# Optimization experiments

Hardware: AMD Instinct MI355X
Metric: run time of the kernel (lower is better)

## Reference

```python
import jax, jax.numpy as jnp
import numpy as np

B = 32768
T = 1024  # num_time_bins


def setup_inputs() -> dict:
    key = jax.random.key(0)
    k1, k2, k3, k4 = jax.random.split(key, 4)
    hazard_values = jax.random.uniform(k1, (B, T), dtype=jnp.float32)
    labels_Y = jax.random.uniform(k2, (B,), dtype=jnp.float32) * T
    # nn.Linear(T, T): weight [T, T] (out, in), bias [T]
    lim = 1.0 / np.sqrt(T)
    W = jax.random.uniform(k3, (T, T), minval=-lim, maxval=lim, dtype=jnp.float32)
    b = jax.random.uniform(k4, (T,), minval=-lim, maxval=lim, dtype=jnp.float32)
    return {"hazard_values": hazard_values, "labels_Y": labels_Y, "W": W, "b": b}


def reference(hazard_values, labels_Y, W, b):
    # linear + sigmoid + argmax -> per-row truncation position
    logits = hazard_values @ W.T + b                       # [B, T]
    trunc_pos = jnp.argmax(jax.nn.sigmoid(logits), axis=1, keepdims=True)  # [B, 1] int
    # survival curve
    S = jnp.cumprod(1.0 - hazard_values, axis=1)           # [B, T]
    # vectorized truncation decay: for t >= p, multiply by exp(-(t - p))
    t = jnp.arange(T)[None, :]                             # [1, T]
    decay = jnp.where(t >= trunc_pos,
                      jnp.exp(-(t - trunc_pos).astype(S.dtype)),
                      jnp.ones((), S.dtype))
    S = S * decay
    # MSE between argmax position and labels (original prints; we skip prints)
    p = trunc_pos[:, 0].astype(jnp.float32)
    truncation_loss = jnp.mean((p - labels_Y) ** 2)
    return trunc_pos, S, truncation_loss
```

## Files before the change

kernel.cpp:

```cpp
#include <hip/hip_runtime.h>

#define B_ROWS 32768
#define T_BINS 1024

typedef __attribute__((ext_vector_type(8))) _Float16 half8;
typedef __attribute__((ext_vector_type(4))) float floatx4;

__device__ __forceinline__ unsigned long long pack_max(float v, int col) {
    unsigned x = __float_as_uint(v);
    x = (x & 0x80000000u) ? ~x : (x | 0x80000000u);
    return ((unsigned long long)x << 32) | (unsigned)(~col);
}

__device__ __forceinline__ void async16(const _Float16* g, _Float16* l) {
    __builtin_amdgcn_global_load_lds(
        (const __attribute__((address_space(1))) unsigned int*)g,
        (__attribute__((address_space(3))) unsigned int*)l,
        16, 0, 0);
}

__global__ __launch_bounds__(256) void tof16_kernel(
    const float* __restrict__ src, _Float16* __restrict__ dst, int n4)
{
    int idx = blockIdx.x * 256 + threadIdx.x;
    if (idx >= n4) return;
    float4 x = ((const float4*)src)[idx];
    union { _Float16 h[4]; ushort4 u; } cv;
    cv.h[0] = (_Float16)x.x;
    cv.h[1] = (_Float16)x.y;
    cv.h[2] = (_Float16)x.z;
    cv.h[3] = (_Float16)x.w;
    ((ushort4*)dst)[idx] = cv.u;
}

__global__ __launch_bounds__(256) void gemm_f16_argmax(
    const _Float16* __restrict__ Ag, const _Float16* __restrict__ Wg,
    const float* __restrict__ bias, unsigned long long* __restrict__ rec)
{
    __shared__ _Float16 sA[128 * 32];
    __shared__ _Float16 sW[128 * 32];

    const int tid  = threadIdx.x;
    const int lane = tid & 63;
    const int wv   = tid >> 6;
    const int wr   = wv >> 1;
    const int wc   = wv & 1;
    const int bx   = blockIdx.x;
    const int by   = blockIdx.y;

    floatx4 acc[4][4];
#pragma unroll
    for (int i = 0; i < 4; ++i)
#pragma unroll
        for (int j = 0; j < 4; ++j) acc[i][j] = (floatx4){0.f, 0.f, 0.f, 0.f};

    const int c0 = tid, c1 = 256 + tid;
    const int r0 = c0 >> 2, kc0 = (c0 & 3) * 8;
    const int r1 = c1 >> 2, kc1 = (c1 & 3) * 8;
    const int ub0 = (wv * 64) * 8;
    const int ub1 = (256 + wv * 64) * 8;

    const size_t a0 = (size_t)(by * 128 + r0) * T_BINS + kc0;
    const size_t a1 = (size_t)(by * 128 + r1) * T_BINS + kc1;
    const size_t w0 = (size_t)(bx * 128 + r0) * T_BINS + kc0;
    const size_t w1 = (size_t)(bx * 128 + r1) * T_BINS + kc1;

    const int ko = (lane >> 4) * 8;

    for (int k0 = 0; k0 < T_BINS; k0 += 32) {
        async16(Ag + a0 + k0, &sA[ub0]);
        async16(Ag + a1 + k0, &sA[ub1]);
        async16(Wg + w0 + k0, &sW[ub0]);
        async16(Wg + w1 + k0, &sW[ub1]);
        asm volatile("s_waitcnt vmcnt(0)" ::: "memory");
        __syncthreads();

        half8 ah[4], wh[4];
#pragma unroll
        for (int i = 0; i < 4; ++i) {
            int ra = (wr * 64 + i * 16 + (lane & 15)) * 32 + ko;
            int rw = (wc * 64 + i * 16 + (lane & 15)) * 32 + ko;
            ah[i] = *(const half8*)&sA[ra];
            wh[i] = *(const half8*)&sW[rw];
        }
#pragma unroll
        for (int i = 0; i < 4; ++i)
#pragma unroll
            for (int j = 0; j < 4; ++j)
                acc[i][j] = __builtin_amdgcn_mfma_f32_16x16x32_f16(ah[i], wh[j], acc[i][j], 0, 0, 0);
        __syncthreads();
    }

    const int colbase = bx * 128 + wc * 64 + (lane & 15);
    float bj[4];
#pragma unroll
    for (int j = 0; j < 4; ++j) bj[j] = bias[colbase + j * 16];

#pragma unroll
    for (int i = 0; i < 4; ++i) {
#pragma unroll
        for (int r = 0; r < 4; ++r) {
            float best = acc[i][0][r] + bj[0];
            int   bc   = colbase;
#pragma unroll
            for (int j = 1; j < 4; ++j) {
                float v = acc[i][j][r] + bj[j];
                if (v > best) { best = v; bc = colbase + j * 16; }
            }
#pragma unroll
            for (int off = 8; off >= 1; off >>= 1) {
                float ov = __shfl_xor(best, off, 64);
                int   oc = __shfl_xor(bc, off, 64);
                if (ov > best || (ov == best && oc < bc)) { best = ov; bc = oc; }
            }
            if ((lane & 15) == 0) {
                int rowG = by * 128 + wr * 64 + i * 16 + (lane >> 4) * 4 + r;
                atomicMax(&rec[rowG], pack_max(best, bc));
            }
        }
    }
}

#define BMf 64
#define BKf 16
#define LDSS (BMf + 4)
__global__ __launch_bounds__(256) void gemm_argmax_fp32(
    const float* __restrict__ A, const float* __restrict__ W,
    const float* __restrict__ bias, unsigned long long* __restrict__ rec)
{
    __shared__ float As[BKf][LDSS];
    __shared__ float Ws[BKf][LDSS];
    const int tid = threadIdx.x;
    const int tx = tid & 15, ty = tid >> 4;
    const int bx = blockIdx.x, by = blockIdx.y;
    const int ar = tid >> 2, ak = (tid & 3) << 2;
    const float* Arow = A + (size_t)(by * BMf + ar) * T_BINS + ak;
    const float* Wrow = W + (size_t)(bx * BMf + ar) * T_BINS + ak;
    float acc[4][4];
#pragma unroll
    for (int i = 0; i < 4; ++i)
#pragma unroll
        for (int j = 0; j < 4; ++j) acc[i][j] = 0.f;
    for (int k0 = 0; k0 < T_BINS; k0 += BKf) {
        float4 av = *(const float4*)(Arow + k0);
        float4 wvv = *(const float4*)(Wrow + k0);
        As[ak + 0][ar] = av.x; As[ak + 1][ar] = av.y; As[ak + 2][ar] = av.z; As[ak + 3][ar] = av.w;
        Ws[ak + 0][ar] = wvv.x; Ws[ak + 1][ar] = wvv.y; Ws[ak + 2][ar] = wvv.z; Ws[ak + 3][ar] = wvv.w;
        __syncthreads();
#pragma unroll
        for (int k = 0; k < BKf; ++k) {
            float4 a4 = *(const float4*)&As[k][ty * 4];
            float4 w4 = *(const float4*)&Ws[k][tx * 4];
            float aa[4] = {a4.x, a4.y, a4.z, a4.w};
            float ww[4] = {w4.x, w4.y, w4.z, w4.w};
#pragma unroll
            for (int i = 0; i < 4; ++i)
#pragma unroll
                for (int j = 0; j < 4; ++j) acc[i][j] = fmaf(aa[i], ww[j], acc[i][j]);
        }
        __syncthreads();
    }
    const int colBase = bx * BMf + tx * 4;
    float bv[4];
#pragma unroll
    for (int j = 0; j < 4; ++j) bv[j] = bias[colBase + j];
#pragma unroll
    for (int i = 0; i < 4; ++i) {
        float best = acc[i][0] + bv[0];
        int bc = colBase;
#pragma unroll
        for (int j = 1; j < 4; ++j) {
            float v = acc[i][j] + bv[j];
            if (v > best) { best = v; bc = colBase + j; }
        }
#pragma unroll
        for (int off = 8; off >= 1; off >>= 1) {
            float ov = __shfl_xor(best, off, 64);
            int oc = __shfl_xor(bc, off, 64);
            if (ov > best || (ov == best && oc < bc)) { best = ov; bc = oc; }
        }
        if (tx == 0) atomicMax(&rec[by * BMf + ty * 4 + i], pack_max(best, bc));
    }
}

__global__ __launch_bounds__(256) void finalize_kernel(
    const unsigned long long* __restrict__ rec, const float* __restrict__ labels,
    float* __restrict__ out_trunc, float* __restrict__ loss_acc)
{
    int i = blockIdx.x * 256 + threadIdx.x;
    unsigned col = ~(unsigned)(rec[i] & 0xFFFFFFFFull);
    float p = (float)col;
    out_trunc[i] = p;
    float d = p - labels[i];
    float term = d * d * (1.0f / (float)B_ROWS);
#pragma unroll
    for (int off = 32; off >= 1; off >>= 1)
        term += __shfl_down(term, off, 64);
    __shared__ float partials[4];
    int lane = threadIdx.x & 63, wv = threadIdx.x >> 6;
    if (lane == 0) partials[wv] = term;
    __syncthreads();
    if (threadIdx.x == 0)
        atomicAdd(loss_acc, partials[0] + partials[1] + partials[2] + partials[3]);
}

__global__ __launch_bounds__(256) void scan_kernel_f16(
    const _Float16* __restrict__ Hh, const float* __restrict__ trunc_f,
    float* __restrict__ Sout)
{
    const int row = blockIdx.x;
    const int tid = threadIdx.x;
    const int lane = tid & 63;
    const int wv = tid >> 6;

    union { ushort4 u; _Float16 h[4]; } cv;
    cv.u = ((const ushort4*)Hh)[(size_t)row * (T_BINS / 4) + tid];
    float l0 = 1.f - (float)cv.h[0];
    float l1 = l0 * (1.f - (float)cv.h[1]);
    float l2 = l1 * (1.f - (float)cv.h[2]);
    float l3 = l2 * (1.f - (float)cv.h[3]);

    float x = l3;
#pragma unroll
    for (int off = 1; off < 64; off <<= 1) {
        float o = __shfl_up(x, off, 64);
        if (lane >= off) x *= o;
    }
    float ex = __shfl_up(x, 1, 64);
    if (lane == 0) ex = 1.f;

    __shared__ float wtot[4];
    if (lane == 63) wtot[wv] = x;
    __syncthreads();
    float wpre = 1.f;
#pragma unroll
    for (int w = 0; w < 3; ++w)
        if (w < wv) wpre *= wtot[w];
    float pre = wpre * ex;

    int p = (int)trunc_f[row];
    int t0 = tid * 4;
    float sv[4] = {pre * l0, pre * l1, pre * l2, pre * l3};
#pragma unroll
    for (int j = 0; j < 4; ++j) {
        int t = t0 + j;
        if (t >= p) sv[j] *= __expf((float)(p - t));
    }
    float4 s4 = {sv[0], sv[1], sv[2], sv[3]};
    *(float4*)(Sout + (size_t)row * T_BINS + tid * 4) = s4;
}

__global__ __launch_bounds__(256) void scan_kernel_f32(
    const float* __restrict__ H, const float* __restrict__ trunc_f,
    float* __restrict__ Sout)
{
    const int row = blockIdx.x;
    const int tid = threadIdx.x;
    const int lane = tid & 63;
    const int wv = tid >> 6;
    const float4 h = *(const float4*)(H + (size_t)row * T_BINS + tid * 4);
    float l0 = 1.f - h.x;
    float l1 = l0 * (1.f - h.y);
    float l2 = l1 * (1.f - h.z);
    float l3 = l2 * (1.f - h.w);
    float x = l3;
#pragma unroll
    for (int off = 1; off < 64; off <<= 1) {
        float o = __shfl_up(x, off, 64);
        if (lane >= off) x *= o;
    }
    float ex = __shfl_up(x, 1, 64);
    if (lane == 0) ex = 1.f;
    __shared__ float wtot[4];
    if (lane == 63) wtot[wv] = x;
    __syncthreads();
    float wpre = 1.f;
#pragma unroll
    for (int w = 0; w < 3; ++w)
        if (w < wv) wpre *= wtot[w];
    float pre = wpre * ex;
    int p = (int)trunc_f[row];
    int t0 = tid * 4;
    float sv[4] = {pre * l0, pre * l1, pre * l2, pre * l3};
#pragma unroll
    for (int j = 0; j < 4; ++j) {
        int t = t0 + j;
        if (t >= p) sv[j] *= __expf((float)(p - t));
    }
    float4 s4 = {sv[0], sv[1], sv[2], sv[3]};
    *(float4*)(Sout + (size_t)row * T_BINS + tid * 4) = s4;
}

extern "C" void kernel_launch(void* const* d_in, const int* in_sizes, int n_in,
                              void* d_out, int out_size, void* d_ws, size_t ws_size,
                              hipStream_t stream)
{
    const float* hazard = (const float*)d_in[0];
    const float* labels = (const float*)d_in[1];
    const float* W      = (const float*)d_in[2];
    const float* bias   = (const float*)d_in[3];

    float* out       = (float*)d_out;
    float* out_trunc = out;
    float* out_S     = out + B_ROWS;
    float* out_loss  = out + B_ROWS + (size_t)B_ROWS * T_BINS;

    unsigned long long* rec = (unsigned long long*)out_S;

    hipMemsetAsync(rec, 0, (size_t)B_ROWS * sizeof(unsigned long long), stream);
    hipMemsetAsync(out_loss, 0, sizeof(float), stream);

    const size_t NA = (size_t)B_ROWS * T_BINS;
    const size_t NW = (size_t)T_BINS * T_BINS;
    const size_t need = (NA + NW) * sizeof(_Float16);

    if (ws_size >= need) {
        _Float16* Ah = (_Float16*)d_ws;
        _Float16* Wh = Ah + NA;
        tof16_kernel<<<(int)(NA / 4 / 256), 256, 0, stream>>>(hazard, Ah, (int)(NA / 4));
        tof16_kernel<<<(int)(NW / 4 / 256), 256, 0, stream>>>(W, Wh, (int)(NW / 4));
        dim3 ggrid(T_BINS / 128, B_ROWS / 128);
        gemm_f16_argmax<<<ggrid, 256, 0, stream>>>(Ah, Wh, bias, rec);
        finalize_kernel<<<B_ROWS / 256, 256, 0, stream>>>(rec, labels, out_trunc, out_loss);
        scan_kernel_f16<<<B_ROWS, 256, 0, stream>>>(Ah, out_trunc, out_S);
    } else {
        dim3 ggrid(T_BINS / BMf, B_ROWS / BMf);
        gemm_argmax_fp32<<<ggrid, 256, 0, stream>>>(hazard, W, bias, rec);
        finalize_kernel<<<B_ROWS / 256, 256, 0, stream>>>(rec, labels, out_trunc, out_loss);
        scan_kernel_f32<<<B_ROWS, 256, 0, stream>>>(hazard, out_trunc, out_S);
    }
}
```

Baseline: 386.1 us.

## Fuse fp16 GEMM, argmax, loss and survival scan into one mega kernel

Replaces the separate passes (fp32→fp16 conversion of hazard values, tiled GEMM with global atomicMax, finalize, and per-row scan) with one kernel per 64-row block. Each block converts its A tile to fp16 on the fly while streaming W, keeps a running argmax across all 1024 output columns, reduces it in shared memory, writes trunc/loss, then computes the cumprod and decay for its rows straight from fp32 hazard values. This removes the full fp16 copy of A, the record memset, global atomics and two extra launches. In exchange the grid is only 512 blocks with a serialized GEMM-then-scan inside each block, and A tiles are re-read once per column chunk, so occupancy and latency hiding may suffer.

```diff
diff --git a/kernel.cpp b/kernel.cpp
--- a/kernel.cpp
+++ b/kernel.cpp
@@ -12,7 +12,7 @@
     return ((unsigned long long)x << 32) | (unsigned)(~col);
 }
 
-__device__ __forceinline__ void async16(const _Float16* g, _Float16* l) {
+__device__ __forceinline__ void async16h(const _Float16* g, _Float16* l) {
     __builtin_amdgcn_global_load_lds(
         (const __attribute__((address_space(1))) unsigned int*)g,
         (__attribute__((address_space(3))) unsigned int*)l,
@@ -33,91 +33,169 @@
     ((ushort4*)dst)[idx] = cv.u;
 }
 
-__global__ __launch_bounds__(256) void gemm_f16_argmax(
-    const _Float16* __restrict__ Ag, const _Float16* __restrict__ Wg,
-    const float* __restrict__ bias, unsigned long long* __restrict__ rec)
-{
-    __shared__ _Float16 sA[128 * 32];
-    __shared__ _Float16 sW[128 * 32];
+__global__ __launch_bounds__(256, 2) void mega_kernel(
+    const float* __restrict__ A, const _Float16* __restrict__ Wh,
+    const float* __restrict__ bias, const float* __restrict__ labels,
+    float* __restrict__ out_trunc, float* __restrict__ out_S,
+    float* __restrict__ loss_acc)
+{
+    __shared__ _Float16 sA[64 * 32];
+    __shared__ _Float16 sW[256 * 32];
+    __shared__ unsigned long long cand[4][64];
+    __shared__ float trunc_s[64];
 
     const int tid  = threadIdx.x;
     const int lane = tid & 63;
-    const int wv   = tid >> 6;
-    const int wr   = wv >> 1;
-    const int wc   = wv & 1;
-    const int bx   = blockIdx.x;
-    const int by   = blockIdx.y;
-
-    floatx4 acc[4][4];
+    const int wc   = tid >> 6;
+    const int by   = blockIdx.x;
+
+    const int arow = tid >> 2;
+    const int akg  = (tid & 3) * 8;
+    const float* Abase = A + (size_t)(by * 64 + arow) * T_BINS + akg;
+    _Float16* sAdst = &sA[arow * 32 + akg];
+
+    const int ko = (lane >> 4) * 8;
+
+    float run_best[4][4];
+    int   run_col[4][4];
 #pragma unroll
     for (int i = 0; i < 4; ++i)
 #pragma unroll
-        for (int j = 0; j < 4; ++j) acc[i][j] = (floatx4){0.f, 0.f, 0.f, 0.f};
-
-    const int c0 = tid, c1 = 256 + tid;
-    const int r0 = c0 >> 2, kc0 = (c0 & 3) * 8;
-    const int r1 = c1 >> 2, kc1 = (c1 & 3) * 8;
-    const int ub0 = (wv * 64) * 8;
-    const int ub1 = (256 + wv * 64) * 8;
-
-    const size_t a0 = (size_t)(by * 128 + r0) * T_BINS + kc0;
-    const size_t a1 = (size_t)(by * 128 + r1) * T_BINS + kc1;
-    const size_t w0 = (size_t)(bx * 128 + r0) * T_BINS + kc0;
-    const size_t w1 = (size_t)(bx * 128 + r1) * T_BINS + kc1;
-
-    const int ko = (lane >> 4) * 8;
-
-    for (int k0 = 0; k0 < T_BINS; k0 += 32) {
-        async16(Ag + a0 + k0, &sA[ub0]);
-        async16(Ag + a1 + k0, &sA[ub1]);
-        async16(Wg + w0 + k0, &sW[ub0]);
-        async16(Wg + w1 + k0, &sW[ub1]);
-        asm volatile("s_waitcnt vmcnt(0)" ::: "memory");
-        __syncthreads();
-
-        half8 ah[4], wh[4];
-#pragma unroll
-        for (int i = 0; i < 4; ++i) {
-            int ra = (wr * 64 + i * 16 + (lane & 15)) * 32 + ko;
-            int rw = (wc * 64 + i * 16 + (lane & 15)) * 32 + ko;
-            ah[i] = *(const half8*)&sA[ra];
-            wh[i] = *(const half8*)&sW[rw];
-        }
+        for (int r = 0; r < 4; ++r) { run_best[i][r] = -3.4e38f; run_col[i][r] = 0; }
+
+    float4 pa0 = *(const float4*)(Abase);
+    float4 pa1 = *(const float4*)(Abase + 4);
+
+    for (int bx = 0; bx < 4; ++bx) {
+        const int colbase = bx * 256 + wc * 64 + (lane & 15);
+        float bj[4];
+#pragma unroll
+        for (int j = 0; j < 4; ++j) bj[j] = bias[colbase + j * 16];
+
+        floatx4 acc[4][4];
 #pragma unroll
         for (int i = 0; i < 4; ++i)
 #pragma unroll
+            for (int j = 0; j < 4; ++j) acc[i][j] = (floatx4){0.f, 0.f, 0.f, 0.f};
+
+        for (int k0 = 0; k0 < T_BINS; k0 += 32) {
+            half8 hv;
+            hv[0] = (_Float16)pa0.x; hv[1] = (_Float16)pa0.y;
+            hv[2] = (_Float16)pa0.z; hv[3] = (_Float16)pa0.w;
+            hv[4] = (_Float16)pa1.x; hv[5] = (_Float16)pa1.y;
+            hv[6] = (_Float16)pa1.z; hv[7] = (_Float16)pa1.w;
+            *(half8*)sAdst = hv;
+#pragma unroll
+            for (int r = 0; r < 4; ++r) {
+                int c = r * 256 + tid;
+                int wrow = c >> 2, wkc = (c & 3) * 8;
+                async16h(Wh + (size_t)(bx * 256 + wrow) * T_BINS + k0 + wkc,
+                         &sW[(r * 256 + wc * 64) * 8]);
+            }
+            int kn = (k0 + 32) & (T_BINS - 1);
+            pa0 = *(const float4*)(Abase + kn);
+            pa1 = *(const float4*)(Abase + kn + 4);
+            asm volatile("s_waitcnt vmcnt(0)" ::: "memory");
+            __syncthreads();
+            half8 ah[4], wh[4];
+#pragma unroll
+            for (int i = 0; i < 4; ++i)
+                ah[i] = *(const half8*)&sA[(i * 16 + (lane & 15)) * 32 + ko];
+#pragma unroll
             for (int j = 0; j < 4; ++j)
-                acc[i][j] = __builtin_amdgcn_mfma_f32_16x16x32_f16(ah[i], wh[j], acc[i][j], 0, 0, 0);
-        __syncthreads();
-    }
-
-    const int colbase = bx * 128 + wc * 64 + (lane & 15);
-    float bj[4];
-#pragma unroll
-    for (int j = 0; j < 4; ++j) bj[j] = bias[colbase + j * 16];
-
-#pragma unroll
-    for (int i = 0; i < 4; ++i) {
+                wh[j] = *(const half8*)&sW[(wc * 64 + j * 16 + (lane & 15)) * 32 + ko];
+#pragma unroll
+            for (int i = 0; i < 4; ++i)
+#pragma unroll
+                for (int j = 0; j < 4; ++j)
+                    acc[i][j] = __builtin_amdgcn_mfma_f32_16x16x32_f16(ah[i], wh[j], acc[i][j], 0, 0, 0);
+            __syncthreads();
+        }
+
+#pragma unroll
+        for (int i = 0; i < 4; ++i)
+#pragma unroll
+            for (int r = 0; r < 4; ++r)
+#pragma unroll
+                for (int j = 0; j < 4; ++j) {
+                    float v = acc[i][j][r] + bj[j];
+                    if (v > run_best[i][r]) { run_best[i][r] = v; run_col[i][r] = colbase + j * 16; }
+                }
+    }
+
+#pragma unroll
+    for (int i = 0; i < 4; ++i)
 #pragma unroll
         for (int r = 0; r < 4; ++r) {
-            float best = acc[i][0][r] + bj[0];
-            int   bc   = colbase;
-#pragma unroll
-            for (int j = 1; j < 4; ++j) {
-                float v = acc[i][j][r] + bj[j];
-                if (v > best) { best = v; bc = colbase + j * 16; }
-            }
+            float best = run_best[i][r];
+            int   bc   = run_col[i][r];
 #pragma unroll
             for (int off = 8; off >= 1; off >>= 1) {
                 float ov = __shfl_xor(best, off, 64);
                 int   oc = __shfl_xor(bc, off, 64);
                 if (ov > best || (ov == best && oc < bc)) { best = ov; bc = oc; }
             }
-            if ((lane & 15) == 0) {
-                int rowG = by * 128 + wr * 64 + i * 16 + (lane >> 4) * 4 + r;
-                atomicMax(&rec[rowG], pack_max(best, bc));
-            }
-        }
+            if ((lane & 15) == 0)
+                cand[wc][i * 16 + (lane >> 4) * 4 + r] = pack_max(best, bc);
+        }
+    __syncthreads();
+
+    if (tid < 64) {
+        unsigned long long m01 = cand[0][tid] > cand[1][tid] ? cand[0][tid] : cand[1][tid];
+        unsigned long long m23 = cand[2][tid] > cand[3][tid] ? cand[2][tid] : cand[3][tid];
+        unsigned long long m = m01 > m23 ? m01 : m23;
+        unsigned col = ~(unsigned)m;
+        float p = (float)col;
+        int rowG = by * 64 + tid;
+        out_trunc[rowG] = p;
+        trunc_s[tid] = p;
+        float d = p - labels[rowG];
+        float term = d * d * (1.0f / (float)B_ROWS);
+#pragma unroll
+        for (int off = 32; off >= 1; off >>= 1)
+            term += __shfl_down(term, off, 64);
+        if (tid == 0) atomicAdd(loss_acc, term);
+    }
+    __syncthreads();
+
+    for (int rr = 0; rr < 16; ++rr) {
+        int row  = wc * 16 + rr;
+        int rowG = by * 64 + row;
+        const float* Hrow = A + (size_t)rowG * T_BINS + lane * 16;
+        float4 h0 = *(const float4*)(Hrow + 0);
+        float4 h1 = *(const float4*)(Hrow + 4);
+        float4 h2 = *(const float4*)(Hrow + 8);
+        float4 h3 = *(const float4*)(Hrow + 12);
+        float hv[16] = {h0.x, h0.y, h0.z, h0.w, h1.x, h1.y, h1.z, h1.w,
+                        h2.x, h2.y, h2.z, h2.w, h3.x, h3.y, h3.z, h3.w};
+        float vprod[16];
+        float run = 1.f;
+#pragma unroll
+        for (int j = 0; j < 16; ++j) { run *= (1.f - hv[j]); vprod[j] = run; }
+        float x = run;
+#pragma unroll
+        for (int off = 1; off < 64; off <<= 1) {
+            float o = __shfl_up(x, off, 64);
+            if (lane >= off) x *= o;
+        }
+        float pre = __shfl_up(x, 1, 64);
+        if (lane == 0) pre = 1.f;
+
+        int p  = (int)trunc_s[row];
+        int t0 = lane * 16;
+        float sv[16];
+#pragma unroll
+        for (int j = 0; j < 16; ++j) {
+            float s = pre * vprod[j];
+            int t = t0 + j;
+            if (t >= p) s *= __expf((float)(p - t));
+            sv[j] = s;
+        }
+        float* Srow = out_S + (size_t)rowG * T_BINS + lane * 16;
+        *(float4*)(Srow + 0)  = (float4){sv[0],  sv[1],  sv[2],  sv[3]};
+        *(float4*)(Srow + 4)  = (float4){sv[4],  sv[5],  sv[6],  sv[7]};
+        *(float4*)(Srow + 8)  = (float4){sv[8],  sv[9],  sv[10], sv[11]};
+        *(float4*)(Srow + 12) = (float4){sv[12], sv[13], sv[14], sv[15]};
     }
 }
 
@@ -202,52 +280,6 @@
     __syncthreads();
     if (threadIdx.x == 0)
         atomicAdd(loss_acc, partials[0] + partials[1] + partials[2] + partials[3]);
-}
-
-__global__ __launch_bounds__(256) void scan_kernel_f16(
-    const _Float16* __restrict__ Hh, const float* __restrict__ trunc_f,
-    float* __restrict__ Sout)
-{
-    const int row = blockIdx.x;
-    const int tid = threadIdx.x;
-    const int lane = tid & 63;
-    const int wv = tid >> 6;
-
-    union { ushort4 u; _Float16 h[4]; } cv;
-    cv.u = ((const ushort4*)Hh)[(size_t)row * (T_BINS / 4) + tid];
-    float l0 = 1.f - (float)cv.h[0];
-    float l1 = l0 * (1.f - (float)cv.h[1]);
-    float l2 = l1 * (1.f - (float)cv.h[2]);
-    float l3 = l2 * (1.f - (float)cv.h[3]);
-
-    float x = l3;
-#pragma unroll
-    for (int off = 1; off < 64; off <<= 1) {
-        float o = __shfl_up(x, off, 64);
-        if (lane >= off) x *= o;
-    }
-    float ex = __shfl_up(x, 1, 64);
-    if (lane == 0) ex = 1.f;
-
-    __shared__ float wtot[4];
-    if (lane == 63) wtot[wv] = x;
-    __syncthreads();
-    float wpre = 1.f;
-#pragma unroll
-    for (int w = 0; w < 3; ++w)
-        if (w < wv) wpre *= wtot[w];
-    float pre = wpre * ex;
-
-    int p = (int)trunc_f[row];
-    int t0 = tid * 4;
-    float sv[4] = {pre * l0, pre * l1, pre * l2, pre * l3};
-#pragma unroll
-    for (int j = 0; j < 4; ++j) {
-        int t = t0 + j;
-        if (t >= p) sv[j] *= __expf((float)(p - t));
-    }
-    float4 s4 = {sv[0], sv[1], sv[2], sv[3]};
-    *(float4*)(Sout + (size_t)row * T_BINS + tid * 4) = s4;
 }
 
 __global__ __launch_bounds__(256) void scan_kernel_f32(
@@ -305,25 +337,17 @@
     float* out_S     = out + B_ROWS;
     float* out_loss  = out + B_ROWS + (size_t)B_ROWS * T_BINS;
 
-    unsigned long long* rec = (unsigned long long*)out_S;
-
-    hipMemsetAsync(rec, 0, (size_t)B_ROWS * sizeof(unsigned long long), stream);
     hipMemsetAsync(out_loss, 0, sizeof(float), stream);
 
-    const size_t NA = (size_t)B_ROWS * T_BINS;
     const size_t NW = (size_t)T_BINS * T_BINS;
-    const size_t need = (NA + NW) * sizeof(_Float16);
-
-    if (ws_size >= need) {
-        _Float16* Ah = (_Float16*)d_ws;
-        _Float16* Wh = Ah + NA;
-        tof16_kernel<<<(int)(NA / 4 / 256), 256, 0, stream>>>(hazard, Ah, (int)(NA / 4));
+    if (ws_size >= NW * sizeof(_Float16)) {
+        _Float16* Wh = (_Float16*)d_ws;
         tof16_kernel<<<(int)(NW / 4 / 256), 256, 0, stream>>>(W, Wh, (int)(NW / 4));
-        dim3 ggrid(T_BINS / 128, B_ROWS / 128);
-        gemm_f16_argmax<<<ggrid, 256, 0, stream>>>(Ah, Wh, bias, rec);
-        finalize_kernel<<<B_ROWS / 256, 256, 0, stream>>>(rec, labels, out_trunc, out_loss);
-        scan_kernel_f16<<<B_ROWS, 256, 0, stream>>>(Ah, out_trunc, out_S);
+        mega_kernel<<<B_ROWS / 64, 256, 0, stream>>>(
+            hazard, Wh, bias, labels, out_trunc, out_S, out_loss);
     } else {
+        unsigned long long* rec = (unsigned long long*)out_S;
+        hipMemsetAsync(rec, 0, (size_t)B_ROWS * sizeof(unsigned long long), stream);
         dim3 ggrid(T_BINS / BMf, B_ROWS / BMf);
         gemm_argmax_fp32<<<ggrid, 256, 0, stream>>>(hazard, W, bias, rec);
         finalize_kernel<<<B_ROWS / 256, 256, 0, stream>>>(rec, labels, out_trunc, out_loss);
```

Result: no change. 379.5 us (-1.7%).
